# Optimization experiments

Measured on AMD Instinct MI355X. Metric: run time of the kernel, lower is better.

The kernel has to match this reference:

```python
import jax, jax.numpy as jnp
import numpy as np

B, T, S, L_SRC, V, H, E, AV = 16, 128, 192, 192, 30522, 768, 768, 200
L_ORG = L_SRC - 1
KEEP, DEL, STOP, PAD = 3, 4, 2, 0  # SP_IDS = [KEEP, DEL, INSERT, STOP, PAD, LEFT, RIGHT, MARK]


def lstm(x, Wih, Whh, bih, bhh):
    # x: [B, T, E] -> outputs [B, T, H]; PyTorch gate order i, f, g, o
    Bx = x.shape[0]
    Hh = Whh.shape[1]
    def step(carry, xt):
        h, c = carry
        g = xt @ Wih.T + bih + h @ Whh.T + bhh
        i, f, gg, o = jnp.split(g, 4, axis=-1)
        c = jax.nn.sigmoid(f) * c + jax.nn.sigmoid(i) * jnp.tanh(gg)
        h = jax.nn.sigmoid(o) * jnp.tanh(c)
        return (h, c), h
    h0 = jnp.zeros((Bx, Hh), x.dtype)
    _, hs = jax.lax.scan(step, (h0, h0), jnp.swapaxes(x, 0, 1))
    return jnp.swapaxes(hs, 0, 1)


def compute_counters(input_edits, org_ids):
    # Vectorized replica of the host-side numpy counter bookkeeping.
    # Emits the PRE-update counters used at each timestep t (updated with gold = input_edits[:, t+1]).
    Bx = input_edits.shape[0]
    golds = jnp.swapaxes(input_edits[:, 1:], 0, 1)  # [T-1, B]
    barange = jnp.arange(Bx)
    Lorg = org_ids.shape[1]
    def step(carry, g):
        cd, ci, ca = carry
        pre = (cd, ci, ca)
        cd2 = cd + ((g == KEEP) | (g == DEL)).astype(jnp.int32)
        alive = (g != DEL) & (g != STOP) & (g != PAD)
        ci2 = ci + alive.astype(jnp.int32)
        nxt = jnp.clip(ca + 1, 0, Lorg - 1)
        tok = org_ids[barange, nxt]
        cond = alive & (g != KEEP) & (ca + 1 < Lorg) & ((tok == 103) | (tok == 3) | (tok == 4))
        ca2 = jnp.where(cond, ca + 1, jnp.maximum(cd2, ca))
        return (cd2, ci2, ca2), pre
    z = jnp.zeros((Bx,), jnp.int32)
    _, (cds, cis, cas) = jax.lax.scan(step, (z, z, z), golds)
    return jnp.swapaxes(cds, 0, 1), jnp.swapaxes(cis, 0, 1), jnp.swapaxes(cas, 0, 1)  # each [B, T-1]


def setup_inputs():
    key = jax.random.key(0)
    ks = jax.random.split(key, 40)
    s = 0.02
    rn = lambda k, sh: jax.random.normal(k, sh, jnp.float32) * s
    inp = {
        "input_edits": jax.random.randint(ks[0], (B, T), 0, 12),
        "input_actions": jax.random.randint(ks[1], (B, T), 0, AV),
        "simp_sent": jax.random.randint(ks[2], (B, S), 0, V),
        "org_ids": jax.random.randint(ks[3], (B, L_ORG), 0, V),
        "encoder_outputs_org": jax.random.normal(ks[4], (B, L_SRC, H), jnp.float32),
        "emb": rn(ks[5], (V, E)),
    }
    i = 6
    for nm in ("e", "a", "w"):
        inp["Wih_" + nm] = rn(ks[i], (4 * H, E)); i += 1
        inp["Whh_" + nm] = rn(ks[i], (4 * H, H)); i += 1
        inp["bih_" + nm] = jnp.zeros((4 * H,), jnp.float32)
        inp["bhh_" + nm] = jnp.zeros((4 * H,), jnp.float32)
    inp["W_align"] = rn(ks[i], (H, H)); i += 1
    inp["W_proj"] = rn(ks[i], (H, H)); i += 1
    inp["W_ref"] = rn(ks[i], (2, H)); i += 1
    inp["b_ref"] = jnp.zeros((2,), jnp.float32)
    inp["W_mlp"] = rn(ks[i], (E, 5 * H)); i += 1
    inp["b_mlp"] = jnp.zeros((E,), jnp.float32)
    inp["W_act"] = rn(ks[i], (E, 5 * H)); i += 1
    inp["b_act"] = jnp.zeros((E,), jnp.float32)
    inp["W_out"] = rn(ks[i], (V, E)); i += 1
    inp["b_out"] = jnp.zeros((V,), jnp.float32)
    inp["W_outact"] = rn(ks[i], (AV, E)); i += 1
    inp["b_outact"] = jnp.zeros((AV,), jnp.float32)
    m = np.full((1, AV), -100000.0, dtype=np.float32)
    m[0, [0, 1, 2, 5, 101, 102]] = 0.0
    inp["action_mask"] = jnp.asarray(m)
    return inp


def reference(input_edits, input_actions, simp_sent, org_ids, encoder_outputs_org, emb,
              Wih_e, Whh_e, bih_e, bhh_e, Wih_a, Whh_a, bih_a, bhh_a, Wih_w, Whh_w, bih_w, bhh_w,
              W_align, W_proj, W_ref, b_ref, W_mlp, b_mlp, W_act, b_act,
              W_out, b_out, W_outact, b_outact, action_mask):
    # tanh(output_hidden_alignment(enc)) then drop the first (CLS) position
    enc = jnp.tanh(encoder_outputs_org @ W_align.T)[:, 1:]  # [B, L_ORG, H]
    out_e = lstm(emb[input_edits], Wih_e, Whh_e, bih_e, bhh_e)
    out_a = lstm(emb[input_actions], Wih_a, Whh_a, bih_a, bhh_a)
    out_w = lstm(emb[simp_sent], Wih_w, Whh_w, bih_w, bhh_w)
    cd, ci, ca = compute_counters(input_edits, org_ids)  # [B, T-1] each
    Tm1 = input_edits.shape[1] - 1
    bidx = jnp.arange(enc.shape[0])[:, None]
    c_input = enc[bidx, cd]   # [B, T-1, H] data-dependent gather per timestep
    c_anno = enc[bidx, ca]
    c_word = out_w[bidx, ci]
    dec_e = out_e[:, :Tm1]
    dec_a = out_a[:, :Tm1]
    c_pair = jnp.stack([c_input, c_anno], axis=2)  # [B, T-1, 2, H]
    wref_e = jax.nn.softmax(dec_e @ W_ref.T + b_ref, axis=-1)
    wref_a = jax.nn.softmax(dec_a @ W_ref.T + b_ref, axis=-1)
    c_edit = jnp.einsum('btk,btkh->bth', wref_e, c_pair)
    c_action = jnp.einsum('btk,btkh->bth', wref_a, c_pair)
    attn = jax.nn.softmax(jnp.einsum('bth,blh->btl', c_word @ W_proj.T, enc), axis=-1)
    applied = jnp.einsum('btl,blh->bth', attn, enc)
    feat_a = jnp.concatenate([dec_a, dec_e, applied, c_action, c_word], axis=-1)
    act_log = jax.nn.log_softmax(jnp.tanh(feat_a @ W_act.T + b_act) @ W_outact.T + b_outact + action_mask[0], axis=-1)
    feat_e = jnp.concatenate([dec_e, dec_a, applied, c_edit, c_word], axis=-1)
    edit_log = jax.nn.log_softmax(jnp.tanh(feat_e @ W_mlp.T + b_mlp) @ W_out.T + b_out, axis=-1)
    return edit_log, act_log
```

## Files before the change

kernel.cpp:

```cpp
#include <hip/hip_runtime.h>
#include <hip/hip_bf16.h>

typedef __hip_bfloat16 bf16;

#define B_    16
#define T_    128
#define S_    192
#define H_    768
#define G4_   3072
#define V_    30522
#define AV_   200
#define L_    191
#define TM1_  127
#define R_    2032
#define K5_   3840
#define NB_   48
#define HSL_  16

typedef short bf16x8_t __attribute__((ext_vector_type(8)));
typedef float f32x4_t  __attribute__((ext_vector_type(4)));

__device__ __forceinline__ float bf2f(bf16 v) { return __bfloat162float(v); }
__device__ __forceinline__ bf16  f2bf(float v) { return __float2bfloat16(v); }
__device__ __forceinline__ unsigned short f2us(float v) { bf16 h = f2bf(v); return *reinterpret_cast<unsigned short*>(&h); }
__device__ __forceinline__ float uslo(unsigned u) { union { unsigned i; float f; } x; x.i = u << 16; return x.f; }
__device__ __forceinline__ float ushi(unsigned u) { union { unsigned i; float f; } x; x.i = u & 0xffff0000u; return x.f; }
__device__ __forceinline__ float us2f(unsigned short u) { union { unsigned i; float f; } x; x.i = ((unsigned)u) << 16; return x.f; }
__device__ __forceinline__ float sigm(float x) { return 1.0f / (1.0f + expf(-x)); }

__device__ __forceinline__ bf16x8_t ld8bf(const bf16* p) { return *(const bf16x8_t*)p; }
__device__ __forceinline__ bf16x8_t ld8bf(const float* p) {
    float4 a = *(const float4*)p;
    float4 b = *(const float4*)(p + 4);
    bf16x8_t r;
    r[0] = (short)f2us(a.x); r[1] = (short)f2us(a.y); r[2] = (short)f2us(a.z); r[3] = (short)f2us(a.w);
    r[4] = (short)f2us(b.x); r[5] = (short)f2us(b.y); r[6] = (short)f2us(b.z); r[7] = (short)f2us(b.w);
    return r;
}

template <typename TA, typename TW>
__global__ __launch_bounds__(256) void gemm_mfma(
    const TA* __restrict__ A, const TW* __restrict__ W,
    const float* __restrict__ bias1, const float* __restrict__ bias2,
    bf16* __restrict__ Ch, float* __restrict__ Cf,
    int M, int N, int K, int act, int rowdiv, int lda)
{
    __shared__ short As[128][40];
    __shared__ short Ws[128][40];
    const int tid = threadIdx.x;
    const int wave = tid >> 6, lane = tid & 63;
    const int mw = (wave >> 1) * 64, nw = (wave & 1) * 64;
    const int bm = blockIdx.x * 128, bn = blockIdx.y * 128;

    const int sr = tid >> 2;
    const int sc = (tid & 3) * 8;

    f32x4_t acc[4][4];
#pragma unroll
    for (int mi = 0; mi < 4; ++mi)
#pragma unroll
        for (int ni = 0; ni < 4; ++ni) acc[mi][ni] = (f32x4_t){0.f, 0.f, 0.f, 0.f};

    const int fr = lane & 15;
    const int fk = (lane >> 4) * 8;

    for (int k0 = 0; k0 < K; k0 += 32) {
#pragma unroll
        for (int c = 0; c < 2; ++c) {
            const int row = sr + c * 64;
            int ga = bm + row; if (ga > M - 1) ga = M - 1;
            const int ra = (rowdiv > 0) ? (ga + ga / rowdiv + 1) : ga;
            *(bf16x8_t*)&As[row][sc] = ld8bf(A + (size_t)ra * lda + k0 + sc);
            int gw = bn + row; if (gw > N - 1) gw = N - 1;
            *(bf16x8_t*)&Ws[row][sc] = ld8bf(W + (size_t)gw * K + k0 + sc);
        }
        __syncthreads();
        bf16x8_t af[4], wf[4];
#pragma unroll
        for (int i = 0; i < 4; ++i) af[i] = *(const bf16x8_t*)&As[mw + i * 16 + fr][fk];
#pragma unroll
        for (int i = 0; i < 4; ++i) wf[i] = *(const bf16x8_t*)&Ws[nw + i * 16 + fr][fk];
#pragma unroll
        for (int mi = 0; mi < 4; ++mi)
#pragma unroll
            for (int ni = 0; ni < 4; ++ni)
                acc[mi][ni] = __builtin_amdgcn_mfma_f32_16x16x32_bf16(af[mi], wf[ni], acc[mi][ni], 0, 0, 0);
        __syncthreads();
    }

    const int cl = lane & 15;
    const int rg = (lane >> 4) * 4;
#pragma unroll
    for (int mi = 0; mi < 4; ++mi) {
#pragma unroll
        for (int ni = 0; ni < 4; ++ni) {
            const int col = bn + nw + ni * 16 + cl;
            if (col >= N) continue;
#pragma unroll
            for (int j = 0; j < 4; ++j) {
                const int row = bm + mw + mi * 16 + rg + j;
                if (row >= M) continue;
                float v = acc[mi][ni][j];
                if (bias1) v += bias1[col];
                if (bias2) v += bias2[col];
                if (act == 1) v = tanhf(v);
                if (Ch) Ch[(size_t)row * N + col] = f2bf(v);
                else    Cf[(size_t)row * N + col] = v;
            }
        }
    }
}

__global__ __launch_bounds__(256) void lstm_mfma_kernel(
    const bf16* __restrict__ pxe, const bf16* __restrict__ pxa, const bf16* __restrict__ pxw,
    const float* __restrict__ We, const float* __restrict__ Wa, const float* __restrict__ Ww,
    bf16* __restrict__ oute, bf16* __restrict__ outa, bf16* __restrict__ outw,
    unsigned short* __restrict__ hbuf, int* __restrict__ flags)
{
    const int which = blockIdx.x / NB_;
    const int nb = blockIdx.x % NB_;
    const bf16* px; const float* W; bf16* out; int Tn;
    if (which == 0)      { px = pxe; W = We; out = oute; Tn = T_; }
    else if (which == 1) { px = pxa; W = Wa; out = outa; Tn = T_; }
    else                 { px = pxw; W = Ww; out = outw; Tn = S_; }
    unsigned short* hG = hbuf + (size_t)which * (2 * B_ * H_);
    int* flg = flags + which * 64;

    const int tid = threadIdx.x;
    const int wv = tid >> 6;
    const int lane = tid & 63;
    const int so = nb * HSL_;

    __shared__ unsigned short hL[16][776];
    __shared__ float gS[4][16][17];
    __shared__ unsigned short oring[8][16][16];

    bf16x8_t Afrag[24];
    {
        const int m = lane & 15;
        const int kb8 = (lane >> 4) * 8;
        const float* wrow = W + (size_t)(wv * H_ + so + m) * H_ + kb8;
#pragma unroll
        for (int kb = 0; kb < 24; ++kb) {
            float4 f0 = *(const float4*)(wrow + kb * 32);
            float4 f1 = *(const float4*)(wrow + kb * 32 + 4);
            bf16x8_t a;
            a[0] = (short)f2us(f0.x); a[1] = (short)f2us(f0.y);
            a[2] = (short)f2us(f0.z); a[3] = (short)f2us(f0.w);
            a[4] = (short)f2us(f1.x); a[5] = (short)f2us(f1.y);
            a[6] = (short)f2us(f1.z); a[7] = (short)f2us(f1.w);
            Afrag[kb] = a;
        }
    }

    for (int i = tid; i < 16 * 776; i += 256) ((unsigned short*)hL)[i] = 0;

    const int cb = tid >> 4;
    const int chl = tid & 15;
    float c = 0.f;

    const int bn = lane & 15;
    const int bk = (lane >> 4) * 8;

    int cur = 0;
    for (int step = 0; step < Tn; ++step) {
        if (step > 0) {
            const unsigned long long* hsrc =
                (const unsigned long long*)(hG + (size_t)cur * (B_ * H_));
            for (int i = tid; i < B_ * H_ / 4; i += 256) {
                const unsigned long long v =
                    __hip_atomic_load(hsrc + i, __ATOMIC_RELAXED, __HIP_MEMORY_SCOPE_AGENT);
                const int bb = i / (H_ / 4);
                const int cc = i - bb * (H_ / 4);
                ((unsigned long long*)&hL[bb][0])[cc] = v;
            }
        }
        __syncthreads();

        f32x4_t acc = {0.f, 0.f, 0.f, 0.f};
#pragma unroll
        for (int kb = 0; kb < 24; ++kb) {
            bf16x8_t bfr = *(const bf16x8_t*)&hL[bn][kb * 32 + bk];
            acc = __builtin_amdgcn_mfma_f32_16x16x32_bf16(Afrag[kb], bfr, acc, 0, 0, 0);
        }
        {
            const int m0 = (lane >> 4) * 4;
#pragma unroll
            for (int j = 0; j < 4; ++j) gS[wv][m0 + j][bn] = acc[j];
        }
        __syncthreads();

        {
            const bf16* pxt = px + ((size_t)cb * Tn + step) * G4_ + so + chl;
            const float gi = gS[0][chl][cb] + bf2f(pxt[0]);
            const float gf = gS[1][chl][cb] + bf2f(pxt[H_]);
            const float gg = gS[2][chl][cb] + bf2f(pxt[2 * H_]);
            const float go = gS[3][chl][cb] + bf2f(pxt[3 * H_]);
            const float cn = sigm(gf) * c + sigm(gi) * tanhf(gg);
            const float hn = sigm(go) * tanhf(cn);
            c = cn;
            oring[step & 7][cb][chl] = f2us(hn);
            __hip_atomic_store(&hG[(size_t)(cur ^ 1) * (B_ * H_) + cb * H_ + so + chl],
                               f2us(hn), __ATOMIC_RELAXED, __HIP_MEMORY_SCOPE_AGENT);
        }
        if ((step & 7) == 7 || step == Tn - 1) {
            const int base = step & ~7;
            const int cnt8 = (step & 7) + 1;
            for (int s2 = 0; s2 < cnt8; ++s2)
                out[((size_t)cb * Tn + base + s2) * H_ + so + chl] =
                    *reinterpret_cast<const bf16*>(&oring[s2][cb][chl]);
        }

        if (step + 1 < Tn) {
            __syncthreads();
            const int target = step + 1;
            if (tid == 0)
                __hip_atomic_store(&flg[nb], target, __ATOMIC_RELAXED, __HIP_MEMORY_SCOPE_AGENT);
            if (tid < 64 && lane < NB_) {
                long guard = 0;
                while (__hip_atomic_load(&flg[lane], __ATOMIC_RELAXED, __HIP_MEMORY_SCOPE_AGENT) < target) {
                    __builtin_amdgcn_s_sleep(1);
                    if (++guard > 50000000L) break;
                }
            }
            __syncthreads();
        }
        cur ^= 1;
    }
}

__global__ void gather_rows_kernel(const int* __restrict__ ids,
                                   const float* __restrict__ emb,
                                   bf16* __restrict__ out)
{
    const int r = blockIdx.x;
    const float4* src = (const float4*)(emb + (size_t)ids[r] * H_);
    ushort4* dst = (ushort4*)(out + (size_t)r * H_);
    for (int h = threadIdx.x; h < H_ / 4; h += 256) {
        float4 v = src[h];
        ushort4 o;
        o.x = f2us(v.x); o.y = f2us(v.y); o.z = f2us(v.z); o.w = f2us(v.w);
        dst[h] = o;
    }
}

__global__ void counters_kernel(const int* __restrict__ edits, const int* __restrict__ org,
                                int* __restrict__ cd, int* __restrict__ ci, int* __restrict__ ca)
{
    const int b = threadIdx.x;
    if (b >= B_) return;
    int vd = 0, vi = 0, va = 0;
    for (int t = 0; t < TM1_; ++t) {
        cd[b * TM1_ + t] = vd; ci[b * TM1_ + t] = vi; ca[b * TM1_ + t] = va;
        const int g = edits[b * T_ + t + 1];
        const int vd2 = vd + ((g == 3 || g == 4) ? 1 : 0);
        const int alive = (g != 4 && g != 2 && g != 0) ? 1 : 0;
        const int vi2 = vi + alive;
        int nxt = va + 1; if (nxt > L_ - 1) nxt = L_ - 1;
        const int tok = org[b * L_ + nxt];
        const bool cond = alive && (g != 3) && (va + 1 < L_) && (tok == 103 || tok == 3 || tok == 4);
        const int va2 = cond ? (va + 1) : max(vd2, va);
        vd = vd2; vi = vi2; va = va2;
    }
}

__global__ void gather_cword_kernel(const bf16* __restrict__ outw, const int* __restrict__ ci,
                                    bf16* __restrict__ cw)
{
    const int r = blockIdx.x;
    const int b = r / TM1_;
    const unsigned* src = (const unsigned*)(outw + ((size_t)b * S_ + ci[r]) * H_);
    unsigned* dst = (unsigned*)(cw + (size_t)r * H_);
    for (int h = threadIdx.x; h < H_ / 2; h += 256) dst[h] = src[h];
}

__global__ __launch_bounds__(256) void ref_combine_kernel(
    const bf16* __restrict__ oute, const bf16* __restrict__ outa, const bf16* __restrict__ enc,
    const float* __restrict__ Wref, const float* __restrict__ bref,
    const int* __restrict__ cd, const int* __restrict__ ca,
    bf16* __restrict__ ced, bf16* __restrict__ cac)
{
    const int r = blockIdx.x;
    const int b = r / TM1_;
    const int t = r % TM1_;
    const bf16* de = oute + ((size_t)b * T_ + t) * H_;
    const bf16* da = outa + ((size_t)b * T_ + t) * H_;
    const int tid = threadIdx.x;
    __shared__ float red[256][4];
    float s0 = 0.f, s1 = 0.f, s2 = 0.f, s3 = 0.f;
    for (int k = tid; k < H_; k += 256) {
        const float w0 = Wref[k];
        const float w1 = Wref[H_ + k];
        const float e = bf2f(de[k]);
        const float a = bf2f(da[k]);
        s0 += e * w0; s1 += e * w1; s2 += a * w0; s3 += a * w1;
    }
    red[tid][0] = s0; red[tid][1] = s1; red[tid][2] = s2; red[tid][3] = s3;
    __syncthreads();
    for (int off = 128; off > 0; off >>= 1) {
        if (tid < off) {
            red[tid][0] += red[tid + off][0];
            red[tid][1] += red[tid + off][1];
            red[tid][2] += red[tid + off][2];
            red[tid][3] += red[tid + off][3];
        }
        __syncthreads();
    }
    const float br0 = bref[0], br1 = bref[1];
    const float xe0 = red[0][0] + br0, xe1 = red[0][1] + br1;
    const float xa0 = red[0][2] + br0, xa1 = red[0][3] + br1;
    const float me = fmaxf(xe0, xe1);
    const float ee0 = expf(xe0 - me), ee1 = expf(xe1 - me);
    const float pe0 = ee0 / (ee0 + ee1), pe1 = ee1 / (ee0 + ee1);
    const float ma = fmaxf(xa0, xa1);
    const float ea0 = expf(xa0 - ma), ea1 = expf(xa1 - ma);
    const float pa0 = ea0 / (ea0 + ea1), pa1 = ea1 / (ea0 + ea1);

    const bf16* ei = enc + ((size_t)b * L_ + cd[r]) * H_;
    const bf16* ea = enc + ((size_t)b * L_ + ca[r]) * H_;
    for (int h = tid; h < H_; h += 256) {
        const float vi = bf2f(ei[h]);
        const float va = bf2f(ea[h]);
        ced[(size_t)r * H_ + h] = f2bf(pe0 * vi + pe1 * va);
        cac[(size_t)r * H_ + h] = f2bf(pa0 * vi + pa1 * va);
    }
}

__global__ __launch_bounds__(256) void attn_kernel(const bf16* __restrict__ q,
                                                   const bf16* __restrict__ enc,
                                                   bf16* __restrict__ app)
{
    const int r = blockIdx.x;
    const int b = r / TM1_;
    const int tid = threadIdx.x;
    __shared__ float qs[H_];
    __shared__ float p[L_ + 1];
    __shared__ float red[256];
    const bf16* qrow = q + (size_t)r * H_;
    for (int h = tid; h < H_; h += 256) qs[h] = bf2f(qrow[h]);
    __syncthreads();
    const bf16* eb = enc + (size_t)b * L_ * H_;
    float myv = -1e30f;
    if (tid < L_) {
        const unsigned* er = (const unsigned*)(eb + (size_t)tid * H_);
        float s = 0.f;
        for (int k2 = 0; k2 < H_ / 2; ++k2) {
            const unsigned u = er[k2];
            s += qs[2 * k2] * uslo(u) + qs[2 * k2 + 1] * ushi(u);
        }
        p[tid] = s;
        myv = s;
    }
    red[tid] = myv;
    __syncthreads();
    for (int off = 128; off > 0; off >>= 1) {
        if (tid < off) red[tid] = fmaxf(red[tid], red[tid + off]);
        __syncthreads();
    }
    const float m = red[0];
    __syncthreads();
    float e = 0.f;
    if (tid < L_) e = expf(p[tid] - m);
    red[tid] = e;
    __syncthreads();
    for (int off = 128; off > 0; off >>= 1) {
        if (tid < off) red[tid] += red[tid + off];
        __syncthreads();
    }
    const float invZ = 1.f / red[0];
    __syncthreads();
    if (tid < L_) p[tid] = e * invZ;
    __syncthreads();
    for (int h = tid; h < H_; h += 256) {
        float s = 0.f;
        for (int l = 0; l < L_; ++l) s += p[l] * bf2f(eb[(size_t)l * H_ + h]);
        app[(size_t)r * H_ + h] = f2bf(s);
    }
}

__global__ void feat_kernel(const bf16* __restrict__ oute, const bf16* __restrict__ outa,
                            const bf16* __restrict__ app, const bf16* __restrict__ ced,
                            const bf16* __restrict__ cac, const bf16* __restrict__ cw,
                            bf16* __restrict__ fe, bf16* __restrict__ fa)
{
    const int r = blockIdx.x;
    const int b = r / TM1_;
    const int t = r % TM1_;
    const unsigned* de  = (const unsigned*)(oute + ((size_t)b * T_ + t) * H_);
    const unsigned* da  = (const unsigned*)(outa + ((size_t)b * T_ + t) * H_);
    const unsigned* ap  = (const unsigned*)(app + (size_t)r * H_);
    const unsigned* ce  = (const unsigned*)(ced + (size_t)r * H_);
    const unsigned* cA  = (const unsigned*)(cac + (size_t)r * H_);
    const unsigned* cwp = (const unsigned*)(cw + (size_t)r * H_);
    unsigned* pfe = (unsigned*)(fe + (size_t)r * K5_);
    unsigned* pfa = (unsigned*)(fa + (size_t)r * K5_);
    const int HW = H_ / 2;
    for (int h = threadIdx.x; h < HW; h += 256) {
        const unsigned ve = de[h], va = da[h], vap = ap[h], vce = ce[h], vca = cA[h], vcw = cwp[h];
        pfe[h] = ve;  pfe[HW + h] = va;  pfe[2 * HW + h] = vap; pfe[3 * HW + h] = vce; pfe[4 * HW + h] = vcw;
        pfa[h] = va;  pfa[HW + h] = ve;  pfa[2 * HW + h] = vap; pfa[3 * HW + h] = vca; pfa[4 * HW + h] = vcw;
    }
}

__global__ __launch_bounds__(1024) void logsoftmax_edit_kernel(float* __restrict__ out)
{
    float* row = out + (size_t)blockIdx.x * V_;
    const int tid = threadIdx.x;
    __shared__ float redm[1024];
    __shared__ float reds[1024];
    float m = -1e30f, s = 0.f;
    for (int i = tid; i < V_; i += 1024) {
        const float x = row[i];
        if (x > m) { s = s * expf(m - x) + 1.f; m = x; }
        else s += expf(x - m);
    }
    redm[tid] = m; reds[tid] = s;
    __syncthreads();
    for (int off = 512; off > 0; off >>= 1) {
        if (tid < off) {
            const float m2 = redm[tid + off], s2 = reds[tid + off];
            const float mn = fmaxf(redm[tid], m2);
            reds[tid] = reds[tid] * expf(redm[tid] - mn) + s2 * expf(m2 - mn);
            redm[tid] = mn;
        }
        __syncthreads();
    }
    const float lz = redm[0] + logf(reds[0]);
    __syncthreads();
    for (int i = tid; i < V_; i += 1024) row[i] = row[i] - lz;
}

__global__ __launch_bounds__(256) void logsoftmax_act_kernel(const float* __restrict__ in,
                                                             float* __restrict__ out)
{
    const float* row = in + (size_t)blockIdx.x * AV_;
    float* orow = out + (size_t)blockIdx.x * AV_;
    const int tid = threadIdx.x;
    __shared__ float red[256];
    float m = -1e30f;
    if (tid < AV_) m = row[tid];
    red[tid] = m;
    __syncthreads();
    for (int off = 128; off > 0; off >>= 1) {
        if (tid < off) red[tid] = fmaxf(red[tid], red[tid + off]);
        __syncthreads();
    }
    m = red[0];
    __syncthreads();
    float s = 0.f;
    if (tid < AV_) s = expf(row[tid] - m);
    red[tid] = s;
    __syncthreads();
    for (int off = 128; off > 0; off >>= 1) {
        if (tid < off) red[tid] += red[tid + off];
        __syncthreads();
    }
    const float lz = m + logf(red[0]);
    if (tid < AV_) orow[tid] = row[tid] - lz;
}

extern "C" void kernel_launch(void* const* d_in, const int* in_sizes, int n_in,
                              void* d_out, int out_size, void* d_ws, size_t ws_size,
                              hipStream_t stream)
{
    const int* input_edits   = (const int*)d_in[0];
    const int* input_actions = (const int*)d_in[1];
    const int* simp_sent     = (const int*)d_in[2];
    const int* org_ids       = (const int*)d_in[3];
    const float* enc_org     = (const float*)d_in[4];
    const float* emb         = (const float*)d_in[5];
    const float* Wih_e = (const float*)d_in[6];
    const float* Whh_e = (const float*)d_in[7];
    const float* bih_e = (const float*)d_in[8];
    const float* bhh_e = (const float*)d_in[9];
    const float* Wih_a = (const float*)d_in[10];
    const float* Whh_a = (const float*)d_in[11];
    const float* bih_a = (const float*)d_in[12];
    const float* bhh_a = (const float*)d_in[13];
    const float* Wih_w = (const float*)d_in[14];
    const float* Whh_w = (const float*)d_in[15];
    const float* bih_w = (const float*)d_in[16];
    const float* bhh_w = (const float*)d_in[17];
    const float* W_align = (const float*)d_in[18];
    const float* W_proj  = (const float*)d_in[19];
    const float* W_ref   = (const float*)d_in[20];
    const float* b_ref   = (const float*)d_in[21];
    const float* W_mlp   = (const float*)d_in[22];
    const float* b_mlp   = (const float*)d_in[23];
    const float* W_act   = (const float*)d_in[24];
    const float* b_act   = (const float*)d_in[25];
    const float* W_out   = (const float*)d_in[26];
    const float* b_out   = (const float*)d_in[27];
    const float* W_outact = (const float*)d_in[28];
    const float* b_outact = (const float*)d_in[29];
    const float* action_mask = (const float*)d_in[30];

    float* out = (float*)d_out;
    float* edit_out = out;
    float* act_out  = out + (size_t)R_ * V_;

    char* p = (char*)d_ws;
    auto take = [&](size_t bytes) { void* q = (void*)p; p += ((bytes + 255) / 256) * 256; return q; };
    int* flags = (int*)take(3 * 256);
    unsigned short* hbuf = (unsigned short*)take((size_t)3 * 2 * B_ * H_ * 2);
    bf16* xe   = (bf16*)take((size_t)B_ * T_ * H_ * 2);
    bf16* xa   = (bf16*)take((size_t)B_ * T_ * H_ * 2);
    bf16* xw   = (bf16*)take((size_t)B_ * S_ * H_ * 2);
    bf16* pxe  = (bf16*)take((size_t)B_ * T_ * G4_ * 2);
    bf16* pxa  = (bf16*)take((size_t)B_ * T_ * G4_ * 2);
    bf16* pxw  = (bf16*)take((size_t)B_ * S_ * G4_ * 2);
    bf16* oute = (bf16*)take((size_t)B_ * T_ * H_ * 2);
    bf16* outa = (bf16*)take((size_t)B_ * T_ * H_ * 2);
    bf16* outw = (bf16*)take((size_t)B_ * S_ * H_ * 2);
    bf16* enc  = (bf16*)take((size_t)B_ * L_ * H_ * 2);
    bf16* cw   = (bf16*)take((size_t)R_ * H_ * 2);
    bf16* ced  = (bf16*)take((size_t)R_ * H_ * 2);
    bf16* cac  = (bf16*)take((size_t)R_ * H_ * 2);
    bf16* qb   = (bf16*)take((size_t)R_ * H_ * 2);
    bf16* app  = (bf16*)take((size_t)R_ * H_ * 2);
    bf16* fe   = (bf16*)take((size_t)R_ * K5_ * 2);
    bf16* fa   = (bf16*)take((size_t)R_ * K5_ * 2);
    bf16* he   = (bf16*)take((size_t)R_ * H_ * 2);
    bf16* ha   = (bf16*)take((size_t)R_ * H_ * 2);
    int*  cd   = (int*)take((size_t)R_ * 4);
    int*  ci   = (int*)take((size_t)R_ * 4);
    int*  ca   = (int*)take((size_t)R_ * 4);
    float* actbuf = (float*)take((size_t)R_ * AV_ * 4);

    hipMemsetAsync(flags, 0, 3 * 256, stream);

    gather_rows_kernel<<<B_ * T_, 256, 0, stream>>>(input_edits, emb, xe);
    gather_rows_kernel<<<B_ * T_, 256, 0, stream>>>(input_actions, emb, xa);
    gather_rows_kernel<<<B_ * S_, 256, 0, stream>>>(simp_sent, emb, xw);

    dim3 gpx((B_ * T_ + 127) / 128, (G4_ + 127) / 128);
    gemm_mfma<bf16, float><<<gpx, 256, 0, stream>>>(xe, Wih_e, bih_e, bhh_e, pxe, nullptr, B_ * T_, G4_, H_, 0, 0, H_);
    gemm_mfma<bf16, float><<<gpx, 256, 0, stream>>>(xa, Wih_a, bih_a, bhh_a, pxa, nullptr, B_ * T_, G4_, H_, 0, 0, H_);
    dim3 gpxw((B_ * S_ + 127) / 128, (G4_ + 127) / 128);
    gemm_mfma<bf16, float><<<gpxw, 256, 0, stream>>>(xw, Wih_w, bih_w, bhh_w, pxw, nullptr, B_ * S_, G4_, H_, 0, 0, H_);

    dim3 genc((B_ * L_ + 127) / 128, (H_ + 127) / 128);
    gemm_mfma<float, float><<<genc, 256, 0, stream>>>(enc_org, W_align, nullptr, nullptr, enc, nullptr, B_ * L_, H_, H_, 1, L_, H_);

    counters_kernel<<<1, 64, 0, stream>>>(input_edits, org_ids, cd, ci, ca);

    lstm_mfma_kernel<<<3 * NB_, 256, 0, stream>>>(pxe, pxa, pxw, Whh_e, Whh_a, Whh_w,
                                                  oute, outa, outw, hbuf, flags);

    gather_cword_kernel<<<R_, 256, 0, stream>>>(outw, ci, cw);

    ref_combine_kernel<<<R_, 256, 0, stream>>>(oute, outa, enc, W_ref, b_ref, cd, ca, ced, cac);

    dim3 gproj((R_ + 127) / 128, (H_ + 127) / 128);
    gemm_mfma<bf16, float><<<gproj, 256, 0, stream>>>(cw, W_proj, nullptr, nullptr, qb, nullptr, R_, H_, H_, 0, 0, H_);

    attn_kernel<<<R_, 256, 0, stream>>>(qb, enc, app);

    feat_kernel<<<R_, 256, 0, stream>>>(oute, outa, app, ced, cac, cw, fe, fa);

    gemm_mfma<bf16, float><<<gproj, 256, 0, stream>>>(fe, W_mlp, b_mlp, nullptr, he, nullptr, R_, H_, K5_, 1, 0, K5_);
    gemm_mfma<bf16, float><<<gproj, 256, 0, stream>>>(fa, W_act, b_act, nullptr, ha, nullptr, R_, H_, K5_, 1, 0, K5_);

    dim3 gact((R_ + 127) / 128, (AV_ + 127) / 128);
    gemm_mfma<bf16, float><<<gact, 256, 0, stream>>>(ha, W_outact, b_outact, action_mask, nullptr, actbuf, R_, AV_, H_, 0, 0, H_);
    logsoftmax_act_kernel<<<R_, 256, 0, stream>>>(actbuf, act_out);

    dim3 gedit((R_ + 127) / 128, (V_ + 127) / 128);
    gemm_mfma<bf16, float><<<gedit, 256, 0, stream>>>(he, W_out, b_out, nullptr, nullptr, edit_out, R_, V_, H_, 0, 0, H_);
    logsoftmax_edit_kernel<<<R_, 1024, 0, stream>>>(edit_out);
}
```

Before: 2.611 ms.

## Pre-convert W_out to bf16, prefetch LSTM gate inputs, streamline edit log-softmax

W_out is converted once to bf16 into a scratch region that aliases the embedding and gate-projection buffers, which are dead after the LSTM. The large vocabulary GEMM then reads bf16 weights instead of converting fp32 on the fly. The LSTM kernel prefetches the next step's precomputed gate inputs during the spin-wait. Each wave now spins on the flags itself, which removes one block barrier per step. The edit log-softmax uses wave-shuffle reductions and keeps the row in LDS as bf16 for the second pass, which saves a global re-read but rounds the output logits to bf16 precision.

```diff
diff --git a/kernel.cpp b/kernel.cpp
--- a/kernel.cpp
+++ b/kernel.cpp
@@ -111,6 +111,16 @@
     }
 }
 
+__global__ void f2b_kernel(const float* __restrict__ in, bf16* __restrict__ out, int n4)
+{
+    const int i = blockIdx.x * 256 + threadIdx.x;
+    if (i >= n4) return;
+    float4 v = *(const float4*)(in + (size_t)i * 4);
+    ushort4 o;
+    o.x = f2us(v.x); o.y = f2us(v.y); o.z = f2us(v.z); o.w = f2us(v.w);
+    *(ushort4*)(out + (size_t)i * 4) = o;
+}
+
 __global__ __launch_bounds__(256) void lstm_mfma_kernel(
     const bf16* __restrict__ pxe, const bf16* __restrict__ pxa, const bf16* __restrict__ pxw,
     const float* __restrict__ We, const float* __restrict__ Wa, const float* __restrict__ Ww,
@@ -161,6 +171,15 @@
 
     const int bn = lane & 15;
     const int bk = (lane >> 4) * 8;
+
+    unsigned short pxr0, pxr1, pxr2, pxr3;
+    {
+        const bf16* q = px + ((size_t)cb * Tn + 0) * G4_ + so + chl;
+        pxr0 = *(const unsigned short*)(q);
+        pxr1 = *(const unsigned short*)(q + H_);
+        pxr2 = *(const unsigned short*)(q + 2 * H_);
+        pxr3 = *(const unsigned short*)(q + 3 * H_);
+    }
 
     int cur = 0;
     for (int step = 0; step < Tn; ++step) {
@@ -191,11 +210,10 @@
         __syncthreads();
 
         {
-            const bf16* pxt = px + ((size_t)cb * Tn + step) * G4_ + so + chl;
-            const float gi = gS[0][chl][cb] + bf2f(pxt[0]);
-            const float gf = gS[1][chl][cb] + bf2f(pxt[H_]);
-            const float gg = gS[2][chl][cb] + bf2f(pxt[2 * H_]);
-            const float go = gS[3][chl][cb] + bf2f(pxt[3 * H_]);
+            const float gi = gS[0][chl][cb] + us2f(pxr0);
+            const float gf = gS[1][chl][cb] + us2f(pxr1);
+            const float gg = gS[2][chl][cb] + us2f(pxr2);
+            const float go = gS[3][chl][cb] + us2f(pxr3);
             const float cn = sigm(gf) * c + sigm(gi) * tanhf(gg);
             const float hn = sigm(go) * tanhf(cn);
             c = cn;
@@ -216,14 +234,20 @@
             const int target = step + 1;
             if (tid == 0)
                 __hip_atomic_store(&flg[nb], target, __ATOMIC_RELAXED, __HIP_MEMORY_SCOPE_AGENT);
-            if (tid < 64 && lane < NB_) {
+            {
+                const bf16* q = px + ((size_t)cb * Tn + target) * G4_ + so + chl;
+                pxr0 = *(const unsigned short*)(q);
+                pxr1 = *(const unsigned short*)(q + H_);
+                pxr2 = *(const unsigned short*)(q + 2 * H_);
+                pxr3 = *(const unsigned short*)(q + 3 * H_);
+            }
+            if (lane < NB_) {
                 long guard = 0;
                 while (__hip_atomic_load(&flg[lane], __ATOMIC_RELAXED, __HIP_MEMORY_SCOPE_AGENT) < target) {
                     __builtin_amdgcn_s_sleep(1);
                     if (++guard > 50000000L) break;
                 }
             }
-            __syncthreads();
         }
         cur ^= 1;
     }
@@ -406,28 +430,45 @@
 {
     float* row = out + (size_t)blockIdx.x * V_;
     const int tid = threadIdx.x;
-    __shared__ float redm[1024];
-    __shared__ float reds[1024];
+    const int lane = tid & 63;
+    const int wid = tid >> 6;
+    __shared__ unsigned short rowb[V_];
+    __shared__ float wredm[16], wreds[16];
+    __shared__ float fin;
+
     float m = -1e30f, s = 0.f;
     for (int i = tid; i < V_; i += 1024) {
         const float x = row[i];
+        rowb[i] = f2us(x);
         if (x > m) { s = s * expf(m - x) + 1.f; m = x; }
         else s += expf(x - m);
     }
-    redm[tid] = m; reds[tid] = s;
-    __syncthreads();
-    for (int off = 512; off > 0; off >>= 1) {
-        if (tid < off) {
-            const float m2 = redm[tid + off], s2 = reds[tid + off];
-            const float mn = fmaxf(redm[tid], m2);
-            reds[tid] = reds[tid] * expf(redm[tid] - mn) + s2 * expf(m2 - mn);
-            redm[tid] = mn;
-        }
-        __syncthreads();
-    }
-    const float lz = redm[0] + logf(reds[0]);
-    __syncthreads();
-    for (int i = tid; i < V_; i += 1024) row[i] = row[i] - lz;
+#pragma unroll
+    for (int off = 32; off > 0; off >>= 1) {
+        const float m2 = __shfl_down(m, off);
+        const float s2 = __shfl_down(s, off);
+        const float mn = fmaxf(m, m2);
+        s = s * expf(m - mn) + s2 * expf(m2 - mn);
+        m = mn;
+    }
+    if (lane == 0) { wredm[wid] = m; wreds[wid] = s; }
+    __syncthreads();
+    if (wid == 0) {
+        m = (lane < 16) ? wredm[lane] : -1e30f;
+        s = (lane < 16) ? wreds[lane] : 0.f;
+#pragma unroll
+        for (int off = 8; off > 0; off >>= 1) {
+            const float m2 = __shfl_down(m, off);
+            const float s2 = __shfl_down(s, off);
+            const float mn = fmaxf(m, m2);
+            s = s * expf(m - mn) + s2 * expf(m2 - mn);
+            m = mn;
+        }
+        if (lane == 0) fin = m + logf(s);
+    }
+    __syncthreads();
+    const float lz = fin;
+    for (int i = tid; i < V_; i += 1024) row[i] = us2f(rowb[i]) - lz;
 }
 
 __global__ __launch_bounds__(256) void logsoftmax_act_kernel(const float* __restrict__ in,
@@ -503,6 +544,7 @@
     auto take = [&](size_t bytes) { void* q = (void*)p; p += ((bytes + 255) / 256) * 256; return q; };
     int* flags = (int*)take(3 * 256);
     unsigned short* hbuf = (unsigned short*)take((size_t)3 * 2 * B_ * H_ * 2);
+    char* alias_base = p;
     bf16* xe   = (bf16*)take((size_t)B_ * T_ * H_ * 2);
     bf16* xa   = (bf16*)take((size_t)B_ * T_ * H_ * 2);
     bf16* xw   = (bf16*)take((size_t)B_ * S_ * H_ * 2);
@@ -526,6 +568,7 @@
     int*  ci   = (int*)take((size_t)R_ * 4);
     int*  ca   = (int*)take((size_t)R_ * 4);
     float* actbuf = (float*)take((size_t)R_ * AV_ * 4);
+    bf16* Wob = (bf16*)alias_base;
 
     hipMemsetAsync(flags, 0, 3 * 256, stream);
 
@@ -547,6 +590,9 @@
     lstm_mfma_kernel<<<3 * NB_, 256, 0, stream>>>(pxe, pxa, pxw, Whh_e, Whh_a, Whh_w,
                                                   oute, outa, outw, hbuf, flags);
 
+    const int nW4 = V_ * H_ / 4;
+    f2b_kernel<<<(nW4 + 255) / 256, 256, 0, stream>>>(W_out, Wob, nW4);
+
     gather_cword_kernel<<<R_, 256, 0, stream>>>(outw, ci, cw);
 
     ref_combine_kernel<<<R_, 256, 0, stream>>>(oute, outa, enc, W_ref, b_ref, cd, ca, ced, cac);
@@ -566,6 +612,6 @@
     logsoftmax_act_kernel<<<R_, 256, 0, stream>>>(actbuf, act_out);
 
     dim3 gedit((R_ + 127) / 128, (V_ + 127) / 128);
-    gemm_mfma<bf16, float><<<gedit, 256, 0, stream>>>(he, W_out, b_out, nullptr, nullptr, edit_out, R_, V_, H_, 0, 0, H_);
+    gemm_mfma<bf16, bf16><<<gedit, 256, 0, stream>>>(he, Wob, b_out, nullptr, nullptr, edit_out, R_, V_, H_, 0, 0, H_);
     logsoftmax_edit_kernel<<<R_, 1024, 0, stream>>>(edit_out);
 }
```

Measured after the change: 2.523 ms. 3.4% less time.
